# Kernel optimization log

Measured on AMD Instinct MI355X. Metric: run time of the kernel, lower is better.

Reference implementation:

```python
import jax, jax.numpy as jnp
import numpy as np

N, E, T = 10000, 50000, 80000   # nodes, edges, triplets
D, H, C, CF = 16, 128, 64, 64   # n_orb, hidden_dim, conv_dim, coeffs_dim


def l2norm(v):
    # matches torch F.normalize(dim=-1): x / max(||x||_2, 1e-12)
    return v / jnp.maximum(jnp.linalg.norm(v, axis=-1, keepdims=True), 1e-12)


def setup_inputs() -> dict:
    key = jax.random.key(0)
    ks = jax.random.split(key, 16)

    def w(k, i, o):
        return jax.random.normal(k, (i, o), jnp.float32) / np.sqrt(i).astype(np.float32)

    return {
        "x": jax.random.normal(ks[0], (N, H), jnp.float32),
        "cji": jax.random.normal(ks[1], (E, D, CF), jnp.float32),
        "robs": jax.random.normal(ks[2], (E, D), jnp.float32),
        "shbs": jax.random.normal(ks[3], (T, D), jnp.float32),
        "idx_i": jax.random.randint(ks[4], (E,), 0, N),
        "idx_j": jax.random.randint(ks[5], (E,), 0, N),
        "tri_idx_k": jax.random.randint(ks[6], (T,), 0, N),
        "edge_idx_kj": jax.random.randint(ks[7], (T,), 0, E),
        "edge_idx_ji": jax.random.randint(ks[8], (T,), 0, E),
        "W_nb": w(ks[9], H, 2 * C), "b_nb": jnp.zeros((2 * C,), jnp.float32),
        "W_c1": w(ks[10], CF, C),
        "W_c2": w(ks[11], C, 2 * C),
        "W_t3": w(ks[12], C, C), "b_t3": jnp.zeros((C,), jnp.float32),
        "W_n1": w(ks[13], 2 * C, C), "b_n1": jnp.zeros((C,), jnp.float32),
        "W_n2": w(ks[14], C, C), "b_n2": jnp.zeros((C,), jnp.float32),
        "W_na": w(ks[15], C, H),
    }


def reference(x, cji, robs, shbs, idx_i, idx_j, tri_idx_k, edge_idx_kj,
              edge_idx_ji, W_nb, b_nb, W_c1, W_c2, W_t3, b_t3, W_n1, b_n1,
              W_n2, b_n2, W_na):
    silu = jax.nn.silu
    # node_before_lin + chunk
    h = x @ W_nb + b_nb                       # [N, 2C]
    xq, xk = jnp.split(h, 2, axis=-1)         # each [N, C]
    # coeffs_before_lin: act -> Dense -> act -> Dense (no biases)
    c = silu(silu(cji) @ W_c1) @ W_c2         # [E, D, 2C]
    cji2, ckj = jnp.split(c, 2, axis=-1)      # each [E, D, C]
    # triplet gathers
    ckj_g = l2norm(ckj[edge_idx_kj])          # [T, D, C]
    tbo = l2norm(jnp.einsum('td,tdh->th', shbs * robs[edge_idx_kj], ckj_g))  # [T, C]
    tbw = tbo * jax.nn.sigmoid(xk[tri_idx_k])  # [T, C]
    # scatter triplets -> edges (dim_size = robs.size(0) = E)
    agg = jax.ops.segment_sum(tbw, edge_idx_ji, num_segments=E)  # [E, C]
    tbw2 = silu(agg) @ W_t3 + b_t3            # three_lin, [E, C]
    cji3 = l2norm(cji2 * (1.0 + tbw2[:, None, :]))  # cji + cji*w, normalized
    lcao = l2norm(jnp.einsum('ed,edh->eh', robs, cji3))  # [E, C]
    # node message: node_lin on concatenated endpoint features
    m = jnp.concatenate([xq[idx_i], xq[idx_j]], axis=-1)  # [E, 2C]
    m = silu(silu(m) @ W_n1 + b_n1) @ W_n2 + b_n2          # [E, C]
    out = x + jax.ops.segment_sum(lcao * m, idx_i, num_segments=N) @ W_na
    return out
```

## Files before the change

kernel.cpp:

```cpp
#include <hip/hip_runtime.h>
#include <hip/hip_bf16.h>

#define NN 10000
#define EE 50000
#define TT 80000
#define DD 16
#define HH 128
#define CC 64

typedef __hip_bfloat16 bf16;
typedef __attribute__((ext_vector_type(8))) short bf16x8;
typedef __attribute__((ext_vector_type(4))) float f32x4;

__device__ __forceinline__ float silu_f(float x) {
  return x * __builtin_amdgcn_rcpf(1.f + __expf(-x));
}
__device__ __forceinline__ float sigm_f(float x) {
  return __builtin_amdgcn_rcpf(1.f + __expf(-x));
}

__device__ __forceinline__ short f2bs(float x) {
  __hip_bfloat16 h = __float2bfloat16(x);
  short s;
  __builtin_memcpy(&s, &h, 2);
  return s;
}

__device__ __forceinline__ float rnorm_f(float ss) {
  return __builtin_amdgcn_rcpf(fmaxf(__builtin_amdgcn_sqrtf(ss), 1e-12f));
}

__device__ __forceinline__ float wave_sum64(float v) {
#pragma unroll
  for (int m = 1; m < 64; m <<= 1) v += __shfl_xor(v, m, 64);
  return v;
}

__device__ __forceinline__ void bf2x(unsigned u, float& lo, float& hi) {
  lo = __uint_as_float(u << 16);
  hi = __uint_as_float(u & 0xffff0000u);
}

#define ZERO_U4 960000
__global__ __launch_bounds__(256) void k_zero(uint4* __restrict__ p) {
  const int stride = gridDim.x * 256;
  for (int i = blockIdx.x * 256 + threadIdx.x; i < ZERO_U4; i += stride)
    p[i] = (uint4){0u, 0u, 0u, 0u};
}

__global__ __launch_bounds__(128) void k_node(
    const float* __restrict__ x, const float* __restrict__ W_nb,
    const float* __restrict__ b_nb, float* __restrict__ sxq,
    float* __restrict__ sigxk) {
  __shared__ float xrow[HH];
  const int n = blockIdx.x;
  const int t = threadIdx.x;
  xrow[t] = x[(size_t)n * HH + t];
  __syncthreads();
  float acc = b_nb[t];
#pragma unroll 8
  for (int k = 0; k < HH; ++k) acc = fmaf(xrow[k], W_nb[k * HH + t], acc);
  if (t < CC)
    sxq[(size_t)n * CC + t] = silu_f(acc);
  else
    sigxk[(size_t)n * CC + (t - CC)] = sigm_f(acc);
}

#define K2_BLOCKS 2048
#define K2_TILES 50000
__global__ __launch_bounds__(256, 2) void k_coeffs(
    const float* __restrict__ cji, const float* __restrict__ W_c1,
    const float* __restrict__ W_c2, bf16* __restrict__ cji2,
    bf16* __restrict__ ckjn) {
  __shared__ __align__(16) short xbuf[4][16 * 72];
  const int tid = threadIdx.x;
  const int w = tid >> 6, l = tid & 63;
  const int lr = l & 15, lg = l >> 4;
  short* mybuf = xbuf[w];

  bf16x8 b1[2][4];
  bf16x8 b2[2][8];
#pragma unroll
  for (int kt = 0; kt < 2; ++kt) {
#pragma unroll
    for (int nt = 0; nt < 4; ++nt) {
      bf16x8 t;
#pragma unroll
      for (int b = 0; b < 8; ++b)
        t[b] = f2bs(W_c1[(kt * 32 + lg * 8 + b) * 64 + nt * 16 + lr]);
      b1[kt][nt] = t;
    }
#pragma unroll
    for (int nt = 0; nt < 8; ++nt) {
      bf16x8 t;
#pragma unroll
      for (int b = 0; b < 8; ++b)
        t[b] = f2bs(W_c2[(kt * 32 + lg * 8 + b) * 128 + nt * 16 + lr]);
      b2[kt][nt] = t;
    }
  }

  const int nwave = K2_BLOCKS * 4;
  int tile = blockIdx.x * 4 + w;
  if (tile >= K2_TILES) return;

  float4 r0, r1, r2, r3;
  {
    const float* Ab = cji + (size_t)tile * 1024 + lr * 64 + lg * 8;
    r0 = *(const float4*)(Ab);
    r1 = *(const float4*)(Ab + 4);
    r2 = *(const float4*)(Ab + 32);
    r3 = *(const float4*)(Ab + 36);
  }

  for (; tile < K2_TILES; tile += nwave) {
    bf16x8 a0, a1;
    a0[0] = f2bs(silu_f(r0.x)); a0[1] = f2bs(silu_f(r0.y));
    a0[2] = f2bs(silu_f(r0.z)); a0[3] = f2bs(silu_f(r0.w));
    a0[4] = f2bs(silu_f(r1.x)); a0[5] = f2bs(silu_f(r1.y));
    a0[6] = f2bs(silu_f(r1.z)); a0[7] = f2bs(silu_f(r1.w));
    a1[0] = f2bs(silu_f(r2.x)); a1[1] = f2bs(silu_f(r2.y));
    a1[2] = f2bs(silu_f(r2.z)); a1[3] = f2bs(silu_f(r2.w));
    a1[4] = f2bs(silu_f(r3.x)); a1[5] = f2bs(silu_f(r3.y));
    a1[6] = f2bs(silu_f(r3.z)); a1[7] = f2bs(silu_f(r3.w));

    const int next = tile + nwave;
    if (next < K2_TILES) {
      const float* Ab = cji + (size_t)next * 1024 + lr * 64 + lg * 8;
      r0 = *(const float4*)(Ab);
      r1 = *(const float4*)(Ab + 4);
      r2 = *(const float4*)(Ab + 32);
      r3 = *(const float4*)(Ab + 36);
    }

    f32x4 acc1[4];
#pragma unroll
    for (int nt = 0; nt < 4; ++nt) acc1[nt] = (f32x4){0.f, 0.f, 0.f, 0.f};
#pragma unroll
    for (int nt = 0; nt < 4; ++nt) {
      acc1[nt] = __builtin_amdgcn_mfma_f32_16x16x32_bf16(a0, b1[0][nt], acc1[nt], 0, 0, 0);
      acc1[nt] = __builtin_amdgcn_mfma_f32_16x16x32_bf16(a1, b1[1][nt], acc1[nt], 0, 0, 0);
    }

#pragma unroll
    for (int nt = 0; nt < 4; ++nt)
#pragma unroll
      for (int j = 0; j < 4; ++j)
        mybuf[(lg * 4 + j) * 72 + nt * 16 + lr] = f2bs(silu_f(acc1[nt][j]));

    const bf16x8 a20 = *(const bf16x8*)(mybuf + lr * 72 + lg * 8);
    const bf16x8 a21 = *(const bf16x8*)(mybuf + lr * 72 + 32 + lg * 8);

    f32x4 acc2[8];
#pragma unroll
    for (int nt = 0; nt < 8; ++nt) acc2[nt] = (f32x4){0.f, 0.f, 0.f, 0.f};
#pragma unroll
    for (int nt = 0; nt < 8; ++nt) {
      acc2[nt] = __builtin_amdgcn_mfma_f32_16x16x32_bf16(a20, b2[0][nt], acc2[nt], 0, 0, 0);
      acc2[nt] = __builtin_amdgcn_mfma_f32_16x16x32_bf16(a21, b2[1][nt], acc2[nt], 0, 0, 0);
    }

    float rn[4];
#pragma unroll
    for (int j = 0; j < 4; ++j) {
      float ss = acc2[4][j] * acc2[4][j];
      ss = fmaf(acc2[5][j], acc2[5][j], ss);
      ss = fmaf(acc2[6][j], acc2[6][j], ss);
      ss = fmaf(acc2[7][j], acc2[7][j], ss);
#pragma unroll
      for (int m = 1; m < 16; m <<= 1) ss += __shfl_xor(ss, m, 64);
      rn[j] = rnorm_f(ss);
    }

    union { short h[16]; uint4 u[2]; } p;
#pragma unroll
    for (int nt = 0; nt < 4; ++nt)
#pragma unroll
      for (int j = 0; j < 4; ++j) p.h[nt * 4 + j] = f2bs(acc2[nt][j]);
    {
      uint4* d0 = (uint4*)(cji2 + (size_t)tile * 1024 + l * 16);
      d0[0] = p.u[0];
      d0[1] = p.u[1];
    }
#pragma unroll
    for (int nt = 0; nt < 4; ++nt)
#pragma unroll
      for (int j = 0; j < 4; ++j) p.h[nt * 4 + j] = f2bs(acc2[4 + nt][j] * rn[j]);
    {
      uint4* d1 = (uint4*)(ckjn + (size_t)tile * 1024 + l * 16);
      d1[0] = p.u[0];
      d1[1] = p.u[1];
    }
  }
}

__global__ __launch_bounds__(256) void k_triplet(
    const bf16* __restrict__ ckjn, const float* __restrict__ shbs,
    const float* __restrict__ robs, const float* __restrict__ sigxk,
    const int* __restrict__ tri_idx_k, const int* __restrict__ edge_idx_kj,
    const int* __restrict__ edge_idx_ji, float* __restrict__ agg) {
  const int wid = (blockIdx.x * 256 + threadIdx.x) >> 6;
  const int l = threadIdx.x & 63;
  if (wid >= TT) return;
  const int lq = l >> 4, lr = l & 15;
  const int kj = edge_idx_kj[wid];
  const int kn = tri_idx_k[wid];
  const int ji = edge_idx_ji[wid];
  const float4 sh = *(const float4*)(shbs + (size_t)wid * DD + lq * 4);
  const float4 rb = *(const float4*)(robs + (size_t)kj * DD + lq * 4);
  const float w0 = sh.x * rb.x, w1 = sh.y * rb.y, w2 = sh.z * rb.z,
              w3 = sh.w * rb.w;
  const uint4* base = (const uint4*)(ckjn + (size_t)kj * 1024 + l * 16);
  const uint4 u0 = base[0], u1 = base[1];
  float acc[4];
  {
    float x0, x1, x2, x3;
    bf2x(u0.x, x0, x1); bf2x(u0.y, x2, x3);
    acc[0] = fmaf(w3, x3, fmaf(w2, x2, fmaf(w1, x1, w0 * x0)));
    bf2x(u0.z, x0, x1); bf2x(u0.w, x2, x3);
    acc[1] = fmaf(w3, x3, fmaf(w2, x2, fmaf(w1, x1, w0 * x0)));
    bf2x(u1.x, x0, x1); bf2x(u1.y, x2, x3);
    acc[2] = fmaf(w3, x3, fmaf(w2, x2, fmaf(w1, x1, w0 * x0)));
    bf2x(u1.z, x0, x1); bf2x(u1.w, x2, x3);
    acc[3] = fmaf(w3, x3, fmaf(w2, x2, fmaf(w1, x1, w0 * x0)));
  }
#pragma unroll
  for (int m = 16; m < 64; m <<= 1)
#pragma unroll
    for (int q = 0; q < 4; ++q) acc[q] += __shfl_xor(acc[q], m, 64);
  const float sel = (lq == 0) ? acc[0] : (lq == 1) ? acc[1] : (lq == 2) ? acc[2] : acc[3];
  const float ss = wave_sum64(sel * sel);
  const float tbw = sel * rnorm_f(ss) * sigxk[(size_t)kn * CC + l];
  atomicAdd(&agg[(size_t)ji * CC + l], tbw);
}

#define K4A_TILES 3125
#define K4A_BLOCKS 256
__global__ __launch_bounds__(256, 2) void k_edge_a(
    const float* __restrict__ agg, const float* __restrict__ sxq,
    const int* __restrict__ idx_i, const int* __restrict__ idx_j,
    const float* __restrict__ W_t3, const float* __restrict__ b_t3,
    const float* __restrict__ W_n1, const float* __restrict__ b_n1,
    const float* __restrict__ W_n2, const float* __restrict__ b_n2,
    float* __restrict__ onew_buf, float* __restrict__ m_buf) {
  __shared__ __align__(16) float fbuf[4][16 * 68];
  __shared__ __align__(16) short sbuf[4][16 * 72];
  const int tid = threadIdx.x;
  const int w = tid >> 6, l = tid & 63;
  const int lr = l & 15, lg = l >> 4;
  float* fb = fbuf[w];
  short* sb = sbuf[w];

  bf16x8 bt3[2][4], bn1[4][4], bn2[2][4];
#pragma unroll
  for (int kt = 0; kt < 2; ++kt)
#pragma unroll
    for (int nt = 0; nt < 4; ++nt) {
      bf16x8 t;
#pragma unroll
      for (int b = 0; b < 8; ++b)
        t[b] = f2bs(W_t3[(kt * 32 + lg * 8 + b) * 64 + nt * 16 + lr]);
      bt3[kt][nt] = t;
    }
#pragma unroll
  for (int kt = 0; kt < 4; ++kt)
#pragma unroll
    for (int nt = 0; nt < 4; ++nt) {
      bf16x8 t;
#pragma unroll
      for (int b = 0; b < 8; ++b)
        t[b] = f2bs(W_n1[(kt * 32 + lg * 8 + b) * 64 + nt * 16 + lr]);
      bn1[kt][nt] = t;
    }
#pragma unroll
  for (int kt = 0; kt < 2; ++kt)
#pragma unroll
    for (int nt = 0; nt < 4; ++nt) {
      bf16x8 t;
#pragma unroll
      for (int b = 0; b < 8; ++b)
        t[b] = f2bs(W_n2[(kt * 32 + lg * 8 + b) * 64 + nt * 16 + lr]);
      bn2[kt][nt] = t;
    }
  float bt3c[4], bn1c[4], bn2c[4];
#pragma unroll
  for (int nt = 0; nt < 4; ++nt) {
    bt3c[nt] = b_t3[nt * 16 + lr];
    bn1c[nt] = b_n1[nt * 16 + lr];
    bn2c[nt] = b_n2[nt * 16 + lr];
  }

  for (int tile = blockIdx.x * 4 + w; tile < K4A_TILES; tile += K4A_BLOCKS * 4) {
    const int e = tile * 16 + lr;
    const int vi = idx_i[e], vj = idx_j[e];

    bf16x8 aagg[2];
#pragma unroll
    for (int kt = 0; kt < 2; ++kt) {
      const float4 u = *(const float4*)(agg + (size_t)e * 64 + kt * 32 + lg * 8);
      const float4 v = *(const float4*)(agg + (size_t)e * 64 + kt * 32 + lg * 8 + 4);
      bf16x8 t;
      t[0] = f2bs(silu_f(u.x)); t[1] = f2bs(silu_f(u.y));
      t[2] = f2bs(silu_f(u.z)); t[3] = f2bs(silu_f(u.w));
      t[4] = f2bs(silu_f(v.x)); t[5] = f2bs(silu_f(v.y));
      t[6] = f2bs(silu_f(v.z)); t[7] = f2bs(silu_f(v.w));
      aagg[kt] = t;
    }
    f32x4 acc[4];
#pragma unroll
    for (int nt = 0; nt < 4; ++nt) acc[nt] = (f32x4){0.f, 0.f, 0.f, 0.f};
#pragma unroll
    for (int nt = 0; nt < 4; ++nt) {
      acc[nt] = __builtin_amdgcn_mfma_f32_16x16x32_bf16(aagg[0], bt3[0][nt], acc[nt], 0, 0, 0);
      acc[nt] = __builtin_amdgcn_mfma_f32_16x16x32_bf16(aagg[1], bt3[1][nt], acc[nt], 0, 0, 0);
    }
#pragma unroll
    for (int nt = 0; nt < 4; ++nt)
#pragma unroll
      for (int j = 0; j < 4; ++j)
        fb[(lg * 4 + j) * 68 + nt * 16 + lr] = 1.f + bt3c[nt] + acc[nt][j];
    {
      const int row = l >> 2, cs = (l & 3) * 16;
      float* dst = onew_buf + (size_t)(tile * 16 + row) * 64 + cs;
#pragma unroll
      for (int q = 0; q < 4; ++q)
        *(float4*)(dst + q * 4) = *(const float4*)(fb + row * 68 + cs + q * 4);
    }

    bf16x8 am[4];
#pragma unroll
    for (int kt = 0; kt < 4; ++kt) {
      const float* src = (kt < 2) ? (sxq + (size_t)vi * 64 + kt * 32)
                                  : (sxq + (size_t)vj * 64 + (kt - 2) * 32);
      const float4 u = *(const float4*)(src + lg * 8);
      const float4 v = *(const float4*)(src + lg * 8 + 4);
      bf16x8 t;
      t[0] = f2bs(u.x); t[1] = f2bs(u.y); t[2] = f2bs(u.z); t[3] = f2bs(u.w);
      t[4] = f2bs(v.x); t[5] = f2bs(v.y); t[6] = f2bs(v.z); t[7] = f2bs(v.w);
      am[kt] = t;
    }
    f32x4 acc1[4];
#pragma unroll
    for (int nt = 0; nt < 4; ++nt) acc1[nt] = (f32x4){0.f, 0.f, 0.f, 0.f};
#pragma unroll
    for (int nt = 0; nt < 4; ++nt)
#pragma unroll
      for (int kt = 0; kt < 4; ++kt)
        acc1[nt] = __builtin_amdgcn_mfma_f32_16x16x32_bf16(am[kt], bn1[kt][nt], acc1[nt], 0, 0, 0);

#pragma unroll
    for (int nt = 0; nt < 4; ++nt)
#pragma unroll
      for (int j = 0; j < 4; ++j)
        sb[(lg * 4 + j) * 72 + nt * 16 + lr] = f2bs(silu_f(acc1[nt][j] + bn1c[nt]));
    const bf16x8 a20 = *(const bf16x8*)(sb + lr * 72 + lg * 8);
    const bf16x8 a21 = *(const bf16x8*)(sb + lr * 72 + 32 + lg * 8);

    f32x4 acc2[4];
#pragma unroll
    for (int nt = 0; nt < 4; ++nt) acc2[nt] = (f32x4){0.f, 0.f, 0.f, 0.f};
#pragma unroll
    for (int nt = 0; nt < 4; ++nt) {
      acc2[nt] = __builtin_amdgcn_mfma_f32_16x16x32_bf16(a20, bn2[0][nt], acc2[nt], 0, 0, 0);
      acc2[nt] = __builtin_amdgcn_mfma_f32_16x16x32_bf16(a21, bn2[1][nt], acc2[nt], 0, 0, 0);
    }
#pragma unroll
    for (int nt = 0; nt < 4; ++nt)
#pragma unroll
      for (int j = 0; j < 4; ++j)
        fb[(lg * 4 + j) * 68 + nt * 16 + lr] = acc2[nt][j] + bn2c[nt];
    {
      const int row = l >> 2, cs = (l & 3) * 16;
      float* dst = m_buf + (size_t)(tile * 16 + row) * 64 + cs;
#pragma unroll
      for (int q = 0; q < 4; ++q)
        *(float4*)(dst + q * 4) = *(const float4*)(fb + row * 68 + cs + q * 4);
    }
  }
}

__global__ __launch_bounds__(256) void k_edge_b(
    const bf16* __restrict__ cji2, const float* __restrict__ robs,
    const float* __restrict__ onew_buf, const float* __restrict__ m_buf,
    const int* __restrict__ idx_i, float* __restrict__ lacc) {
  const int wid = (blockIdx.x * 256 + threadIdx.x) >> 6;
  const int l = threadIdx.x & 63;
  if (wid >= EE) return;
  const int lq = l >> 4, lr = l & 15;
  const uint4* base = (const uint4*)(cji2 + (size_t)wid * 1024 + l * 16);
  const uint4 u0 = base[0], u1 = base[1];
  const float* ob = onew_buf + (size_t)wid * 64 + lr;
  const float ow0 = ob[0], ow1 = ob[16], ow2 = ob[32], ow3 = ob[48];
  float v[16];
  bf2x(u0.x, v[0], v[1]);  bf2x(u0.y, v[2], v[3]);
  bf2x(u0.z, v[4], v[5]);  bf2x(u0.w, v[6], v[7]);
  bf2x(u1.x, v[8], v[9]);  bf2x(u1.y, v[10], v[11]);
  bf2x(u1.z, v[12], v[13]); bf2x(u1.w, v[14], v[15]);
#pragma unroll
  for (int j = 0; j < 4; ++j) {
    v[j] *= ow0; v[4 + j] *= ow1; v[8 + j] *= ow2; v[12 + j] *= ow3;
  }
  float sq[4];
#pragma unroll
  for (int j = 0; j < 4; ++j)
    sq[j] = fmaf(v[j], v[j],
            fmaf(v[4 + j], v[4 + j],
            fmaf(v[8 + j], v[8 + j], v[12 + j] * v[12 + j])));
#pragma unroll
  for (int m = 1; m < 16; m <<= 1)
#pragma unroll
    for (int j = 0; j < 4; ++j) sq[j] += __shfl_xor(sq[j], m, 64);
  const float4 rb = *(const float4*)(robs + (size_t)wid * DD + lq * 4);
  const float t0 = rb.x * rnorm_f(sq[0]), t1 = rb.y * rnorm_f(sq[1]),
              t2 = rb.z * rnorm_f(sq[2]), t3 = rb.w * rnorm_f(sq[3]);
  float lcq[4];
#pragma unroll
  for (int q = 0; q < 4; ++q)
    lcq[q] = fmaf(t0, v[q * 4 + 0],
             fmaf(t1, v[q * 4 + 1],
             fmaf(t2, v[q * 4 + 2], t3 * v[q * 4 + 3])));
#pragma unroll
  for (int m = 16; m < 64; m <<= 1)
#pragma unroll
    for (int q = 0; q < 4; ++q) lcq[q] += __shfl_xor(lcq[q], m, 64);
  const float sel = (lq == 0) ? lcq[0] : (lq == 1) ? lcq[1] : (lq == 2) ? lcq[2] : lcq[3];
  const float ss = wave_sum64(sel * sel);
  const float lcao = sel * rnorm_f(ss);
  atomicAdd(&lacc[(size_t)idx_i[wid] * CC + l],
            lcao * m_buf[(size_t)wid * 64 + l]);
}

__global__ __launch_bounds__(128) void k_out(
    const float* __restrict__ x, const float* __restrict__ lacc,
    const float* __restrict__ W_na, float* __restrict__ out) {
  __shared__ float lrow[CC];
  const int n = blockIdx.x;
  const int t = threadIdx.x;
  if (t < CC) lrow[t] = lacc[(size_t)n * CC + t];
  __syncthreads();
  float acc = x[(size_t)n * HH + t];
#pragma unroll 8
  for (int k = 0; k < CC; ++k) acc = fmaf(lrow[k], W_na[k * HH + t], acc);
  out[(size_t)n * HH + t] = acc;
}

extern "C" void kernel_launch(void* const* d_in, const int* in_sizes, int n_in,
                              void* d_out, int out_size, void* d_ws,
                              size_t ws_size, hipStream_t stream) {
  const float* x = (const float*)d_in[0];
  const float* cji = (const float*)d_in[1];
  const float* robs = (const float*)d_in[2];
  const float* shbs = (const float*)d_in[3];
  const int* idx_i = (const int*)d_in[4];
  const int* idx_j = (const int*)d_in[5];
  const int* tri_idx_k = (const int*)d_in[6];
  const int* edge_idx_kj = (const int*)d_in[7];
  const int* edge_idx_ji = (const int*)d_in[8];
  const float* W_nb = (const float*)d_in[9];
  const float* b_nb = (const float*)d_in[10];
  const float* W_c1 = (const float*)d_in[11];
  const float* W_c2 = (const float*)d_in[12];
  const float* W_t3 = (const float*)d_in[13];
  const float* b_t3 = (const float*)d_in[14];
  const float* W_n1 = (const float*)d_in[15];
  const float* b_n1 = (const float*)d_in[16];
  const float* W_n2 = (const float*)d_in[17];
  const float* b_n2 = (const float*)d_in[18];
  const float* W_na = (const float*)d_in[19];
  float* out = (float*)d_out;

  char* ws = (char*)d_ws;
  const size_t NC4 = (size_t)NN * CC * 4;
  const size_t EDC2 = (size_t)EE * DD * CC * 2;
  const size_t EC4 = (size_t)EE * CC * 4;
  float* sxq = (float*)(ws);
  float* sigxk = (float*)(ws + NC4);
  bf16* cji2 = (bf16*)(ws + 2 * NC4);
  bf16* ckjn = (bf16*)(ws + 2 * NC4 + EDC2);
  float* agg = (float*)(ws + 2 * NC4 + 2 * EDC2);
  float* lacc = (float*)(ws + 2 * NC4 + 2 * EDC2 + EC4);
  float* onew_buf = (float*)(ws + 2 * NC4 + EDC2);
  float* m_buf = (float*)(ws + 2 * NC4 + EDC2 + EC4);

  k_zero<<<1024, 256, 0, stream>>>((uint4*)agg);

  k_node<<<NN, 128, 0, stream>>>(x, W_nb, b_nb, sxq, sigxk);
  k_coeffs<<<K2_BLOCKS, 256, 0, stream>>>(cji, W_c1, W_c2, cji2, ckjn);
  k_triplet<<<(TT + 3) / 4, 256, 0, stream>>>(ckjn, shbs, robs, sigxk,
                                              tri_idx_k, edge_idx_kj,
                                              edge_idx_ji, agg);
  k_edge_a<<<K4A_BLOCKS, 256, 0, stream>>>(
      agg, sxq, idx_i, idx_j, W_t3, b_t3, W_n1, b_n1, W_n2, b_n2, onew_buf,
      m_buf);
  k_edge_b<<<EE / 4, 256, 0, stream>>>(cji2, robs, onew_buf, m_buf, idx_i,
                                       lacc);
  k_out<<<NN, 128, 0, stream>>>(x, lacc, W_na, out);
}
```

Measured before the change: 220.5 us.

## Batch multiple rows/triplets/edges per block or wave to raise ILP and reuse

k_node and k_out now process 8 nodes per block, so each weight load from global memory is reused across 8 rows staged in shared memory. k_triplet handles 4 triplets per wave and k_edge_b handles 2 edges per wave, issuing all gathers up front and interleaving the shuffle reductions to hide latency. The cost is higher register pressure, which can lower occupancy, and fewer blocks launched.

```diff
diff --git a/kernel.cpp b/kernel.cpp
--- a/kernel.cpp
+++ b/kernel.cpp
@@ -30,12 +30,6 @@
   return __builtin_amdgcn_rcpf(fmaxf(__builtin_amdgcn_sqrtf(ss), 1e-12f));
 }
 
-__device__ __forceinline__ float wave_sum64(float v) {
-#pragma unroll
-  for (int m = 1; m < 64; m <<= 1) v += __shfl_xor(v, m, 64);
-  return v;
-}
-
 __device__ __forceinline__ void bf2x(unsigned u, float& lo, float& hi) {
   lo = __uint_as_float(u << 16);
   hi = __uint_as_float(u & 0xffff0000u);
@@ -52,18 +46,39 @@
     const float* __restrict__ x, const float* __restrict__ W_nb,
     const float* __restrict__ b_nb, float* __restrict__ sxq,
     float* __restrict__ sigxk) {
-  __shared__ float xrow[HH];
-  const int n = blockIdx.x;
+  __shared__ __align__(16) float xs[8][HH];
   const int t = threadIdx.x;
-  xrow[t] = x[(size_t)n * HH + t];
+  const int base = blockIdx.x * 8;
+#pragma unroll
+  for (int i = 0; i < 8; ++i) xs[i][t] = x[(size_t)(base + i) * HH + t];
   __syncthreads();
-  float acc = b_nb[t];
-#pragma unroll 8
-  for (int k = 0; k < HH; ++k) acc = fmaf(xrow[k], W_nb[k * HH + t], acc);
-  if (t < CC)
-    sxq[(size_t)n * CC + t] = silu_f(acc);
-  else
-    sigxk[(size_t)n * CC + (t - CC)] = sigm_f(acc);
+  float acc[8];
+  const float bb = b_nb[t];
+#pragma unroll
+  for (int i = 0; i < 8; ++i) acc[i] = bb;
+  for (int k = 0; k < HH; k += 4) {
+    const float w0 = W_nb[(k + 0) * HH + t];
+    const float w1 = W_nb[(k + 1) * HH + t];
+    const float w2 = W_nb[(k + 2) * HH + t];
+    const float w3 = W_nb[(k + 3) * HH + t];
+#pragma unroll
+    for (int i = 0; i < 8; ++i) {
+      const float4 xv = *(const float4*)(&xs[i][k]);
+      acc[i] = fmaf(xv.x, w0, acc[i]);
+      acc[i] = fmaf(xv.y, w1, acc[i]);
+      acc[i] = fmaf(xv.z, w2, acc[i]);
+      acc[i] = fmaf(xv.w, w3, acc[i]);
+    }
+  }
+  if (t < CC) {
+#pragma unroll
+    for (int i = 0; i < 8; ++i)
+      sxq[(size_t)(base + i) * CC + t] = silu_f(acc[i]);
+  } else {
+#pragma unroll
+    for (int i = 0; i < 8; ++i)
+      sigxk[(size_t)(base + i) * CC + (t - CC)] = sigm_f(acc[i]);
+  }
 }
 
 #define K2_BLOCKS 2048
@@ -194,6 +209,7 @@
   }
 }
 
+#define K3_WAVES 20000
 __global__ __launch_bounds__(256) void k_triplet(
     const bf16* __restrict__ ckjn, const float* __restrict__ shbs,
     const float* __restrict__ robs, const float* __restrict__ sigxk,
@@ -201,37 +217,68 @@
     const int* __restrict__ edge_idx_ji, float* __restrict__ agg) {
   const int wid = (blockIdx.x * 256 + threadIdx.x) >> 6;
   const int l = threadIdx.x & 63;
-  if (wid >= TT) return;
-  const int lq = l >> 4, lr = l & 15;
-  const int kj = edge_idx_kj[wid];
-  const int kn = tri_idx_k[wid];
-  const int ji = edge_idx_ji[wid];
-  const float4 sh = *(const float4*)(shbs + (size_t)wid * DD + lq * 4);
-  const float4 rb = *(const float4*)(robs + (size_t)kj * DD + lq * 4);
-  const float w0 = sh.x * rb.x, w1 = sh.y * rb.y, w2 = sh.z * rb.z,
-              w3 = sh.w * rb.w;
-  const uint4* base = (const uint4*)(ckjn + (size_t)kj * 1024 + l * 16);
-  const uint4 u0 = base[0], u1 = base[1];
-  float acc[4];
-  {
+  if (wid >= K3_WAVES) return;
+  const int lq = l >> 4;
+  const int t0 = wid * 4;
+
+  int kj[4], kn[4], ji[4];
+#pragma unroll
+  for (int i = 0; i < 4; ++i) {
+    kj[i] = edge_idx_kj[t0 + i];
+    kn[i] = tri_idx_k[t0 + i];
+    ji[i] = edge_idx_ji[t0 + i];
+  }
+  float4 sh[4], rb[4];
+  uint4 u0[4], u1[4];
+  float sx[4];
+#pragma unroll
+  for (int i = 0; i < 4; ++i) {
+    sh[i] = *(const float4*)(shbs + (size_t)(t0 + i) * DD + lq * 4);
+    rb[i] = *(const float4*)(robs + (size_t)kj[i] * DD + lq * 4);
+    const uint4* b = (const uint4*)(ckjn + (size_t)kj[i] * 1024 + l * 16);
+    u0[i] = b[0];
+    u1[i] = b[1];
+    sx[i] = sigxk[(size_t)kn[i] * CC + l];
+  }
+
+  float acc[4][4];
+#pragma unroll
+  for (int i = 0; i < 4; ++i) {
+    const float w0 = sh[i].x * rb[i].x, w1 = sh[i].y * rb[i].y,
+                w2 = sh[i].z * rb[i].z, w3 = sh[i].w * rb[i].w;
     float x0, x1, x2, x3;
-    bf2x(u0.x, x0, x1); bf2x(u0.y, x2, x3);
-    acc[0] = fmaf(w3, x3, fmaf(w2, x2, fmaf(w1, x1, w0 * x0)));
-    bf2x(u0.z, x0, x1); bf2x(u0.w, x2, x3);
-    acc[1] = fmaf(w3, x3, fmaf(w2, x2, fmaf(w1, x1, w0 * x0)));
-    bf2x(u1.x, x0, x1); bf2x(u1.y, x2, x3);
-    acc[2] = fmaf(w3, x3, fmaf(w2, x2, fmaf(w1, x1, w0 * x0)));
-    bf2x(u1.z, x0, x1); bf2x(u1.w, x2, x3);
-    acc[3] = fmaf(w3, x3, fmaf(w2, x2, fmaf(w1, x1, w0 * x0)));
+    bf2x(u0[i].x, x0, x1); bf2x(u0[i].y, x2, x3);
+    acc[i][0] = fmaf(w3, x3, fmaf(w2, x2, fmaf(w1, x1, w0 * x0)));
+    bf2x(u0[i].z, x0, x1); bf2x(u0[i].w, x2, x3);
+    acc[i][1] = fmaf(w3, x3, fmaf(w2, x2, fmaf(w1, x1, w0 * x0)));
+    bf2x(u1[i].x, x0, x1); bf2x(u1[i].y, x2, x3);
+    acc[i][2] = fmaf(w3, x3, fmaf(w2, x2, fmaf(w1, x1, w0 * x0)));
+    bf2x(u1[i].z, x0, x1); bf2x(u1[i].w, x2, x3);
+    acc[i][3] = fmaf(w3, x3, fmaf(w2, x2, fmaf(w1, x1, w0 * x0)));
   }
 #pragma unroll
   for (int m = 16; m < 64; m <<= 1)
 #pragma unroll
-    for (int q = 0; q < 4; ++q) acc[q] += __shfl_xor(acc[q], m, 64);
-  const float sel = (lq == 0) ? acc[0] : (lq == 1) ? acc[1] : (lq == 2) ? acc[2] : acc[3];
-  const float ss = wave_sum64(sel * sel);
-  const float tbw = sel * rnorm_f(ss) * sigxk[(size_t)kn * CC + l];
-  atomicAdd(&agg[(size_t)ji * CC + l], tbw);
+    for (int i = 0; i < 4; ++i)
+#pragma unroll
+      for (int q = 0; q < 4; ++q) acc[i][q] += __shfl_xor(acc[i][q], m, 64);
+
+  float sel[4], ss[4];
+#pragma unroll
+  for (int i = 0; i < 4; ++i) {
+    sel[i] = (lq == 0) ? acc[i][0] : (lq == 1) ? acc[i][1]
+             : (lq == 2) ? acc[i][2] : acc[i][3];
+    ss[i] = sel[i] * sel[i];
+  }
+#pragma unroll
+  for (int m = 1; m < 64; m <<= 1)
+#pragma unroll
+    for (int i = 0; i < 4; ++i) ss[i] += __shfl_xor(ss[i], m, 64);
+#pragma unroll
+  for (int i = 0; i < 4; ++i) {
+    const float tbw = sel[i] * rnorm_f(ss[i]) * sx[i];
+    atomicAdd(&agg[(size_t)ji[i] * CC + l], tbw);
+  }
 }
 
 #define K4A_TILES 3125
@@ -379,69 +426,129 @@
   }
 }
 
+#define K4B_WAVES 25000
 __global__ __launch_bounds__(256) void k_edge_b(
     const bf16* __restrict__ cji2, const float* __restrict__ robs,
     const float* __restrict__ onew_buf, const float* __restrict__ m_buf,
     const int* __restrict__ idx_i, float* __restrict__ lacc) {
   const int wid = (blockIdx.x * 256 + threadIdx.x) >> 6;
   const int l = threadIdx.x & 63;
-  if (wid >= EE) return;
+  if (wid >= K4B_WAVES) return;
   const int lq = l >> 4, lr = l & 15;
-  const uint4* base = (const uint4*)(cji2 + (size_t)wid * 1024 + l * 16);
-  const uint4 u0 = base[0], u1 = base[1];
-  const float* ob = onew_buf + (size_t)wid * 64 + lr;
-  const float ow0 = ob[0], ow1 = ob[16], ow2 = ob[32], ow3 = ob[48];
-  float v[16];
-  bf2x(u0.x, v[0], v[1]);  bf2x(u0.y, v[2], v[3]);
-  bf2x(u0.z, v[4], v[5]);  bf2x(u0.w, v[6], v[7]);
-  bf2x(u1.x, v[8], v[9]);  bf2x(u1.y, v[10], v[11]);
-  bf2x(u1.z, v[12], v[13]); bf2x(u1.w, v[14], v[15]);
-#pragma unroll
-  for (int j = 0; j < 4; ++j) {
-    v[j] *= ow0; v[4 + j] *= ow1; v[8 + j] *= ow2; v[12 + j] *= ow3;
-  }
-  float sq[4];
-#pragma unroll
-  for (int j = 0; j < 4; ++j)
-    sq[j] = fmaf(v[j], v[j],
-            fmaf(v[4 + j], v[4 + j],
-            fmaf(v[8 + j], v[8 + j], v[12 + j] * v[12 + j])));
+  const int e0 = wid * 2;
+
+  uint4 u0[2], u1[2];
+  float4 rb[2];
+  float ow[2][4], mm[2];
+  int vi[2];
+#pragma unroll
+  for (int i = 0; i < 2; ++i) {
+    const uint4* base = (const uint4*)(cji2 + (size_t)(e0 + i) * 1024 + l * 16);
+    u0[i] = base[0];
+    u1[i] = base[1];
+    const float* ob = onew_buf + (size_t)(e0 + i) * 64 + lr;
+    ow[i][0] = ob[0]; ow[i][1] = ob[16]; ow[i][2] = ob[32]; ow[i][3] = ob[48];
+    rb[i] = *(const float4*)(robs + (size_t)(e0 + i) * DD + lq * 4);
+    mm[i] = m_buf[(size_t)(e0 + i) * 64 + l];
+    vi[i] = idx_i[e0 + i];
+  }
+
+  float v[2][16];
+#pragma unroll
+  for (int i = 0; i < 2; ++i) {
+    bf2x(u0[i].x, v[i][0], v[i][1]);   bf2x(u0[i].y, v[i][2], v[i][3]);
+    bf2x(u0[i].z, v[i][4], v[i][5]);   bf2x(u0[i].w, v[i][6], v[i][7]);
+    bf2x(u1[i].x, v[i][8], v[i][9]);   bf2x(u1[i].y, v[i][10], v[i][11]);
+    bf2x(u1[i].z, v[i][12], v[i][13]); bf2x(u1[i].w, v[i][14], v[i][15]);
+#pragma unroll
+    for (int j = 0; j < 4; ++j) {
+      v[i][j] *= ow[i][0];
+      v[i][4 + j] *= ow[i][1];
+      v[i][8 + j] *= ow[i][2];
+      v[i][12 + j] *= ow[i][3];
+    }
+  }
+  float sq[2][4];
+#pragma unroll
+  for (int i = 0; i < 2; ++i)
+#pragma unroll
+    for (int j = 0; j < 4; ++j)
+      sq[i][j] = fmaf(v[i][j], v[i][j],
+                 fmaf(v[i][4 + j], v[i][4 + j],
+                 fmaf(v[i][8 + j], v[i][8 + j], v[i][12 + j] * v[i][12 + j])));
 #pragma unroll
   for (int m = 1; m < 16; m <<= 1)
 #pragma unroll
-    for (int j = 0; j < 4; ++j) sq[j] += __shfl_xor(sq[j], m, 64);
-  const float4 rb = *(const float4*)(robs + (size_t)wid * DD + lq * 4);
-  const float t0 = rb.x * rnorm_f(sq[0]), t1 = rb.y * rnorm_f(sq[1]),
-              t2 = rb.z * rnorm_f(sq[2]), t3 = rb.w * rnorm_f(sq[3]);
-  float lcq[4];
-#pragma unroll
-  for (int q = 0; q < 4; ++q)
-    lcq[q] = fmaf(t0, v[q * 4 + 0],
-             fmaf(t1, v[q * 4 + 1],
-             fmaf(t2, v[q * 4 + 2], t3 * v[q * 4 + 3])));
+    for (int i = 0; i < 2; ++i)
+#pragma unroll
+      for (int j = 0; j < 4; ++j) sq[i][j] += __shfl_xor(sq[i][j], m, 64);
+
+  float lcq[2][4];
+#pragma unroll
+  for (int i = 0; i < 2; ++i) {
+    const float t0 = rb[i].x * rnorm_f(sq[i][0]),
+                t1 = rb[i].y * rnorm_f(sq[i][1]),
+                t2 = rb[i].z * rnorm_f(sq[i][2]),
+                t3 = rb[i].w * rnorm_f(sq[i][3]);
+#pragma unroll
+    for (int q = 0; q < 4; ++q)
+      lcq[i][q] = fmaf(t0, v[i][q * 4 + 0],
+                  fmaf(t1, v[i][q * 4 + 1],
+                  fmaf(t2, v[i][q * 4 + 2], t3 * v[i][q * 4 + 3])));
+  }
 #pragma unroll
   for (int m = 16; m < 64; m <<= 1)
 #pragma unroll
-    for (int q = 0; q < 4; ++q) lcq[q] += __shfl_xor(lcq[q], m, 64);
-  const float sel = (lq == 0) ? lcq[0] : (lq == 1) ? lcq[1] : (lq == 2) ? lcq[2] : lcq[3];
-  const float ss = wave_sum64(sel * sel);
-  const float lcao = sel * rnorm_f(ss);
-  atomicAdd(&lacc[(size_t)idx_i[wid] * CC + l],
-            lcao * m_buf[(size_t)wid * 64 + l]);
+    for (int i = 0; i < 2; ++i)
+#pragma unroll
+      for (int q = 0; q < 4; ++q) lcq[i][q] += __shfl_xor(lcq[i][q], m, 64);
+
+  float sel[2], ss[2];
+#pragma unroll
+  for (int i = 0; i < 2; ++i) {
+    sel[i] = (lq == 0) ? lcq[i][0] : (lq == 1) ? lcq[i][1]
+             : (lq == 2) ? lcq[i][2] : lcq[i][3];
+    ss[i] = sel[i] * sel[i];
+  }
+#pragma unroll
+  for (int m = 1; m < 64; m <<= 1)
+#pragma unroll
+    for (int i = 0; i < 2; ++i) ss[i] += __shfl_xor(ss[i], m, 64);
+#pragma unroll
+  for (int i = 0; i < 2; ++i) {
+    const float lcao = sel[i] * rnorm_f(ss[i]);
+    atomicAdd(&lacc[(size_t)vi[i] * CC + l], lcao * mm[i]);
+  }
 }
 
 __global__ __launch_bounds__(128) void k_out(
     const float* __restrict__ x, const float* __restrict__ lacc,
     const float* __restrict__ W_na, float* __restrict__ out) {
-  __shared__ float lrow[CC];
-  const int n = blockIdx.x;
+  __shared__ __align__(16) float ls[8][CC];
   const int t = threadIdx.x;
-  if (t < CC) lrow[t] = lacc[(size_t)n * CC + t];
+  const int base = blockIdx.x * 8;
+  for (int idx = t; idx < 8 * CC; idx += 128)
+    ls[idx >> 6][idx & 63] = lacc[(size_t)(base + (idx >> 6)) * CC + (idx & 63)];
   __syncthreads();
-  float acc = x[(size_t)n * HH + t];
-#pragma unroll 8
-  for (int k = 0; k < CC; ++k) acc = fmaf(lrow[k], W_na[k * HH + t], acc);
-  out[(size_t)n * HH + t] = acc;
+  float acc[8];
+#pragma unroll
+  for (int i = 0; i < 8; ++i) acc[i] = x[(size_t)(base + i) * HH + t];
+  for (int k = 0; k < CC; k += 4) {
+    const float w0 = W_na[(k + 0) * HH + t];
+    const float w1 = W_na[(k + 1) * HH + t];
+    const float w2 = W_na[(k + 2) * HH + t];
+    const float w3 = W_na[(k + 3) * HH + t];
+#pragma unroll
+    for (int i = 0; i < 8; ++i) {
+      const float4 lv = *(const float4*)(&ls[i][k]);
+      acc[i] = fmaf(lv.x, w0, acc[i]);
+      acc[i] = fmaf(lv.y, w1, acc[i]);
+      acc[i] = fmaf(lv.z, w2, acc[i]);
+      acc[i] = fmaf(lv.w, w3, acc[i]);
+    }
+  }
+#pragma unroll
+  for (int i = 0; i < 8; ++i) out[(size_t)(base + i) * HH + t] = acc[i];
 }
 
 extern "C" void kernel_launch(void* const* d_in, const int* in_sizes, int n_in,
@@ -484,15 +591,15 @@
 
   k_zero<<<1024, 256, 0, stream>>>((uint4*)agg);
 
-  k_node<<<NN, 128, 0, stream>>>(x, W_nb, b_nb, sxq, sigxk);
+  k_node<<<NN / 8, 128, 0, stream>>>(x, W_nb, b_nb, sxq, sigxk);
   k_coeffs<<<K2_BLOCKS, 256, 0, stream>>>(cji, W_c1, W_c2, cji2, ckjn);
-  k_triplet<<<(TT + 3) / 4, 256, 0, stream>>>(ckjn, shbs, robs, sigxk,
-                                              tri_idx_k, edge_idx_kj,
-                                              edge_idx_ji, agg);
+  k_triplet<<<(K3_WAVES + 3) / 4, 256, 0, stream>>>(ckjn, shbs, robs, sigxk,
+                                                    tri_idx_k, edge_idx_kj,
+                                                    edge_idx_ji, agg);
   k_edge_a<<<K4A_BLOCKS, 256, 0, stream>>>(
       agg, sxq, idx_i, idx_j, W_t3, b_t3, W_n1, b_n1, W_n2, b_n2, onew_buf,
       m_buf);
-  k_edge_b<<<EE / 4, 256, 0, stream>>>(cji2, robs, onew_buf, m_buf, idx_i,
-                                       lacc);
-  k_out<<<NN, 128, 0, stream>>>(x, lacc, W_na, out);
-}
+  k_edge_b<<<(K4B_WAVES + 3) / 4, 256, 0, stream>>>(cji2, robs, onew_buf,
+                                                    m_buf, idx_i, lacc);
+  k_out<<<NN / 8, 128, 0, stream>>>(x, lacc, W_na, out);
+}
```

Result: faster. 200.4 us (-9.1%).
